# Kernel tuning notes

Hardware: AMD Instinct MI355X
Metric: run time of the kernel (lower is better)

The kernel has to match this reference:

```python
import jax, jax.numpy as jnp
import numpy as np

B, N, PLANE, H, W = 2, 6, 64, 48, 48
HIDP = 64
PS = 3
RATES = 3


def conv2d(x, w, b, pad, dil=1):
    # x: [BN, Cin, H, W], w: [Cout, Cin, kh, kw]
    out = jax.lax.conv_general_dilated(
        x, w, window_strides=(1, 1),
        padding=[(pad, pad), (pad, pad)],
        rhs_dilation=(dil, dil),
        dimension_numbers=('NCHW', 'OIHW', 'NCHW'))
    return out + b[None, :, None, None]


def avgpool3(x):
    bn, c, h, w = x.shape
    return x.reshape(bn, c, h // PS, PS, w // PS, PS).mean(axis=(3, 5))


def setup_inputs() -> dict:
    key = jax.random.key(0)
    ks = jax.random.split(key, 20)
    s = 0.05
    hid_pa = PLANE * 3  # 192, hidden width of MultiFieldConv2d
    d = {
        'x': jax.random.normal(ks[0], (B, N, PLANE, H, W), jnp.float32),
        # patch_aggr: 3 dilated convs (rates 1..3), k=3, plane -> plane*3
        'pa_w1': jax.random.normal(ks[1], (hid_pa, PLANE, 3, 3)) * s,
        'pa_b1': jnp.zeros((hid_pa,)),
        'pa_w2': jax.random.normal(ks[2], (hid_pa, PLANE, 3, 3)) * s,
        'pa_b2': jnp.zeros((hid_pa,)),
        'pa_w3': jax.random.normal(ks[3], (hid_pa, PLANE, 3, 3)) * s,
        'pa_b3': jnp.zeros((hid_pa,)),
        # convert: 1x1 (hid_pa*rates -> 3*hidp), relu, 1x1 (3*hidp -> 3*hidp)
        'pa_cw1': jax.random.normal(ks[4], (3 * HIDP, hid_pa * RATES, 1, 1)) * s,
        'pa_cb1': jnp.zeros((3 * HIDP,)),
        'pa_cw2': jax.random.normal(ks[5], (3 * HIDP, 3 * HIDP, 1, 1)) * s,
        'pa_cb2': jnp.zeros((3 * HIDP,)),
        # to_kv conv: k=3 pad=1, hidp -> hidp
        'kv_w': jax.random.normal(ks[6], (HIDP, HIDP, 3, 3)) * s,
        'kv_b': jnp.zeros((HIDP,)),
        # to_out: 1x1 hidp->plane, relu, 1x1 plane->plane, relu
        'out_w1': jax.random.normal(ks[7], (PLANE, HIDP, 1, 1)) * s,
        'out_b1': jnp.zeros((PLANE,)),
        'out_w2': jax.random.normal(ks[8], (PLANE, PLANE, 1, 1)) * s,
        'out_b2': jnp.zeros((PLANE,)),
        'scales': jnp.ones((N,)),
    }
    return d


def reference(x, pa_w1, pa_b1, pa_w2, pa_b2, pa_w3, pa_b3,
              pa_cw1, pa_cb1, pa_cw2, pa_cb2,
              kv_w, kv_b, out_w1, out_b1, out_w2, out_b2, scales):
    b, n, c, h, w = x.shape
    scale = HIDP ** (-0.5)
    xf = x.reshape(b * n, c, h, w)

    # MultiFieldConv2d: dilated convs (same spatial size for odd k), concat, 1x1 convert
    u = jnp.concatenate([
        conv2d(xf, pa_w1, pa_b1, pad=1, dil=1),
        conv2d(xf, pa_w2, pa_b2, pad=2, dil=2),
        conv2d(xf, pa_w3, pa_b3, pad=3, dil=3),
    ], axis=1)
    qkv = conv2d(jax.nn.relu(conv2d(u, pa_cw1, pa_cb1, 0)), pa_cw2, pa_cb2, 0)
    qkv = jax.nn.relu(qkv)  # F.relu(patch_aggr(x))
    xq, xk, xv = jnp.split(qkv, 3, axis=1)  # each [BN, hidp, H, W]

    def to_kv(t):
        return avgpool3(jax.nn.relu(conv2d(t, kv_w, kv_b, pad=PS // 2)))

    k_ = to_kv(xk)                       # [BN, hidp, H/3, W/3]
    v_ = to_kv(xv) * (1.0 / PS ** 2)

    hw_kv = k_.shape[2] * k_.shape[3]
    Qs = xq.reshape(b, n, HIDP, h * w).transpose(0, 1, 3, 2)   # b n g d
    Ks = k_.reshape(b, n, HIDP, hw_kv).transpose(0, 1, 3, 2)   # b m k d
    Vs = v_.reshape(b, n, HIDP, hw_kv).transpose(0, 1, 3, 2)

    # Leave-one-out sigmoid attention: sum_{j != i} sigmoid(q_i k_j^T * scale) @ v_j
    # Computed as full sum minus the self (j == i) term (exact same math).
    A_all = jax.nn.sigmoid(jnp.einsum('bngd,bmkd->bngmk', Qs, Ks) * scale)
    out_all = jnp.einsum('bngmk,bmkd->bngd', A_all, Vs)
    A_self = jax.nn.sigmoid(jnp.einsum('bngd,bnkd->bngk', Qs, Ks) * scale)
    out_self = jnp.einsum('bngk,bnkd->bngd', A_self, Vs)
    attn_out = out_all - out_self                               # [b, n, HW, hidp]

    res = attn_out.transpose(0, 1, 3, 2).reshape(b, n, HIDP, h, w)
    xv5 = xv.reshape(b, n, HIDP, h, w)
    res = jax.nn.relu(res + scales[None, :, None, None, None] * xv5)

    rf = res.reshape(b * n, HIDP, h, w)
    o = jax.nn.relu(conv2d(jax.nn.relu(conv2d(rf, out_w1, out_b1, 0)), out_w2, out_b2, 0))
    return o.reshape(b, n, c, h, w)
```

## Files before the change

kernel.cpp:

```cpp
#include <hip/hip_runtime.h>
#include <hip/hip_bf16.h>
#include <math.h>

#define BB 2
#define NVIEW 6
#define BN 12
#define CIN 64
#define HH 48
#define WW 48
#define PP (HH*WW)
#define OC 192
#define HPA 192
#define HIDP 64
#define KHW 16
#define PK 256
#define PADW 54
#define PADA (PADW*PADW)
#define NTOT (BN*PP)
#define K1 1728
#define KVPW 50
#define KVPA (KVPW*KVPW)

typedef __attribute__((ext_vector_type(8))) short bf16x8;
typedef __attribute__((ext_vector_type(4))) float f32x4;

#define OFF_WEFFB 0
#define SZ_WEFFB_FL (OC*K1/2)
#define OFF_BEFF (OFF_WEFFB + SZ_WEFFB_FL)
#define SZ_BEFF 256
#define OFF_CW2B (OFF_BEFF + SZ_BEFF)
#define SZ_CW2B_FL (OC*OC/2)
#define OFF_WKVB (OFF_CW2B + SZ_CW2B_FL)
#define SZ_WKVB_FL (64*576/2)
#define OFF_PADXT (OFF_WKVB + SZ_WKVB_FL)
#define SZ_PADXT_FL (BN*PADA*64/2)
#define OFF_QB16 (OFF_PADXT + SZ_PADXT_FL)
#define SZ_QB16_FL (BN*PP*64/2)
#define OFF_KB16 (OFF_QB16 + SZ_QB16_FL)
#define SZ_KB16_FL (BN*PK*64/2)
#define OFF_VB16T (OFF_KB16 + SZ_KB16_FL)
#define SZ_VB16T_FL (BN*64*PK/2)
#define OFF_KVPAD (OFF_VB16T + SZ_VB16T_FL)
#define SZ_KVPAD_FL (BN*2*KVPA*64/2)
#define OFF_CONVB (OFF_KVPAD + SZ_KVPAD_FL)
#define SZ_CONVB_FL (BN*2*PP*64/2)
#define OFF_W1SW (OFF_CONVB + SZ_CONVB_FL)
#define SZ_WSW_FL 2048
#define OFF_W2SW (OFF_W1SW + SZ_WSW_FL)
#define OFF_ATTNP (OFF_W2SW + SZ_WSW_FL)
#define SZ_ATTNP (BN*PP*HIDP)
#define OFF_XVB16 (OFF_ATTNP + 2*SZ_ATTNP)
#define SZ_XVB16_FL (BN*PP*64/2)

__device__ __forceinline__ void load_lds16(const void* g, void* l) {
    __builtin_amdgcn_global_load_lds(
        (const __attribute__((address_space(1))) unsigned int*)g,
        (__attribute__((address_space(3))) unsigned int*)l, 16, 0, 0);
}

__device__ __forceinline__ unsigned short f2bu(float f) {
    __hip_bfloat16 h = __float2bfloat16(f);
    return *(unsigned short*)&h;
}

__device__ __forceinline__ float bu2f(unsigned short h) {
    unsigned int u = ((unsigned int)h) << 16;
    return *(float*)&u;
}

__global__ __launch_bounds__(192) void k_fold(const float* __restrict__ cw1,
                       const float* __restrict__ cb1,
                       const float* __restrict__ w1, const float* __restrict__ b1,
                       const float* __restrict__ w2, const float* __restrict__ b2,
                       const float* __restrict__ w3, const float* __restrict__ b3,
                       __hip_bfloat16* __restrict__ weffb, float* __restrict__ beff) {
    __shared__ float cw1s[8][HPA];
    int b = blockIdx.x;
    int r = b / 72;
    int rem = b % 72;
    int og = rem / 3, tz = rem % 3;
    int tid = threadIdx.x;
    int tg = tz*192 + tid;
    int ic = tg / 9, tap = tg % 9;
    const float* w = (r==0) ? w1 : (r==1) ? w2 : w3;
    #pragma unroll
    for (int j = 0; j < 8; ++j)
        cw1s[j][tid] = cw1[(size_t)(og*8+j)*(HPA*3) + r*HPA + tid];
    __syncthreads();
    float acc[8] = {0,0,0,0,0,0,0,0};
    for (int c = 0; c < HPA; ++c) {
        float wv = w[(size_t)c*(CIN*9) + tg];
        #pragma unroll
        for (int j = 0; j < 8; ++j)
            acc[j] += cw1s[j][c] * wv;
    }
    #pragma unroll
    for (int j = 0; j < 8; ++j)
        weffb[(size_t)(og*8+j)*K1 + r*576 + tap*64 + ic] = __float2bfloat16(acc[j]);
    if (r == 0 && tz == 0 && tid < 8) {
        int o = og*8 + tid;
        float bacc = cb1[o];
        for (int rr = 0; rr < 3; ++rr) {
            const float* bb = (rr==0)?b1:(rr==1)?b2:b3;
            for (int c = 0; c < HPA; ++c)
                bacc += cw1[(size_t)o*(HPA*3) + rr*HPA + c] * bb[c];
        }
        beff[o] = bacc;
    }
}

__global__ void k_wprep(const float* __restrict__ kvw, const float* __restrict__ cw2,
                        const float* __restrict__ w1, const float* __restrict__ w2,
                        __hip_bfloat16* __restrict__ wkvb, __hip_bfloat16* __restrict__ cw2b,
                        __hip_bfloat16* __restrict__ w1sw, __hip_bfloat16* __restrict__ w2sw,
                        __hip_bfloat16* __restrict__ kvpad) {
    int idx = blockIdx.x*256 + threadIdx.x;
    if (idx < 36864) {
        int oc = idx / 576, rest = idx % 576;
        int tap = rest / 64, ic = rest % 64;
        wkvb[idx] = __float2bfloat16(kvw[(oc*64 + ic)*9 + tap]);
    } else if (idx < 73728) {
        int i = idx - 36864;
        cw2b[i] = __float2bfloat16(cw2[i]);
    } else if (idx < 81920) {
        int i = idx - 73728;
        const float* w = (i < 4096) ? w1 : w2;
        __hip_bfloat16* dst = (i < 4096) ? w1sw : w2sw;
        int j = i & 4095;
        int oc = j >> 6, s = (j >> 3) & 7, e = j & 7;
        int k = ((s ^ (oc & 7)) << 3) + e;
        dst[j] = __float2bfloat16(w[oc*64 + k]);
    } else if (idx < 86624) {
        int i = idx - 81920;
        int bn2 = i / 196, h = i % 196;
        int py, px;
        if (h < 50)       { py = 0;        px = h; }
        else if (h < 100) { py = 49;       px = h - 50; }
        else if (h < 148) { py = h - 99;   px = 0; }
        else              { py = h - 147;  px = 49; }
        bf16x8 z = (bf16x8){0,0,0,0,0,0,0,0};
        __hip_bfloat16* dst = kvpad + ((size_t)bn2*KVPA + py*KVPW + px)*64;
        #pragma unroll
        for (int j = 0; j < 8; ++j) *(bf16x8*)(dst + j*8) = z;
    }
}

__global__ void k_padxT(const float* __restrict__ x, __hip_bfloat16* __restrict__ padxT) {
    int idx = blockIdx.x*256 + threadIdx.x;
    if (idx >= BN*PADA) return;
    int spos = idx % PADA; int bn = idx / PADA;
    int sy = spos / PADW, sx = spos % PADW;
    __hip_bfloat16* dst = padxT + (size_t)idx*64;
    if (sy >= 3 && sy < 51 && sx >= 3 && sx < 51) {
        const float* src = x + (size_t)bn*CIN*PP + (sy-3)*WW + (sx-3);
        #pragma unroll 8
        for (int ic = 0; ic < 64; ++ic) dst[ic] = __float2bfloat16(src[ic*PP]);
    } else {
        #pragma unroll 8
        for (int ic = 0; ic < 64; ++ic) dst[ic] = __float2bfloat16(0.f);
    }
}

__global__ __launch_bounds__(256) void k_mfc(const __hip_bfloat16* __restrict__ wA,
        const __hip_bfloat16* __restrict__ pxT, const __hip_bfloat16* __restrict__ cw2b,
        const float* __restrict__ beff, const float* __restrict__ cb2,
        __hip_bfloat16* __restrict__ xvb16, __hip_bfloat16* __restrict__ qb16,
        __hip_bfloat16* __restrict__ kvpad) {
    __shared__ __align__(16) char smem[65536];
    int tid = threadIdx.x;
    int wid = tid >> 6, lane = tid & 63;
    int bn = blockIdx.x / 36;
    int pb = (blockIdx.x % 36) * 64;
    int sgr = ((lane&7) ^ (lane>>3)) * 8;
    int l7 = lane & 7, lh = lane >> 4, rrow = lane & 15, gcol = lane >> 4;

    size_t gbase[8];
    int dbase[8];
    #pragma unroll
    for (int s2 = 0; s2 < 8; ++s2) {
        int seg = wid*8 + s2;
        if (seg < 24) {
            int row = seg*8 + (lane>>3);
            gbase[s2] = (size_t)row*K1 + sgr;
            dbase[s2] = seg*1024;
        } else {
            int p = pb + (seg-24)*8 + (lane>>3);
            int py = p / WW, px = p % WW;
            gbase[s2] = ((size_t)bn*PADA + (py+3)*PADW + (px+3))*64 + sgr;
            dbase[s2] = 49152 + (seg-24)*1024;
        }
    }

    auto stage1 = [&](int kt, int par) {
        int r_ = kt / 9, tap = kt - r_*9;
        int doff = (r_+1)*((tap/3 - 1)*PADW + (tap%3 - 1));
        int poA = par ? 24576 : 0;
        int poB = par ? 8192 : 0;
        #pragma unroll
        for (int s2 = 0; s2 < 8; ++s2) {
            int seg = wid*8 + s2;
            const __hip_bfloat16* g = (seg < 24) ? wA + gbase[s2] + kt*64
                                                 : pxT + gbase[s2] + (size_t)doff*64;
            load_lds16(g, smem + dbase[s2] + ((seg < 24) ? poA : poB));
        }
    };

    f32x4 acc1[3][4];
    #pragma unroll
    for (int m = 0; m < 3; ++m)
        #pragma unroll
        for (int nf = 0; nf < 4; ++nf) acc1[m][nf] = (f32x4){0.f,0.f,0.f,0.f};

    stage1(0, 0);
    __syncthreads();
    for (int kt = 0; kt < 27; ++kt) {
        int par = kt & 1;
        if (kt < 26) stage1(kt+1, par^1);
        int aB = par ? 24576 : 0;
        int bB = 49152 + (par ? 8192 : 0);
        bf16x8 a[3][2], b[4][2];
        #pragma unroll
        for (int kk = 0; kk < 2; ++kk) {
            int gof = ((kk*4 + lh) ^ l7) << 4;
            #pragma unroll
            for (int m = 0; m < 3; ++m)
                a[m][kk] = *(const bf16x8*)(smem + aB + (wid*48 + m*16 + rrow)*128 + gof);
            #pragma unroll
            for (int nf = 0; nf < 4; ++nf)
                b[nf][kk] = *(const bf16x8*)(smem + bB + (nf*16 + rrow)*128 + gof);
        }
        #pragma unroll
        for (int kk = 0; kk < 2; ++kk)
            #pragma unroll
            for (int m = 0; m < 3; ++m)
                #pragma unroll
                for (int nf = 0; nf < 4; ++nf)
                    acc1[m][nf] = __builtin_amdgcn_mfma_f32_16x16x32_bf16(
                        a[m][kk], b[nf][kk], acc1[m][nf], 0, 0, 0);
        __syncthreads();
    }

    f32x4 acc2[3][4];
    #pragma unroll
    for (int m = 0; m < 3; ++m)
        #pragma unroll
        for (int nf = 0; nf < 4; ++nf) acc2[m][nf] = (f32x4){0.f,0.f,0.f,0.f};

    for (int kt2 = 0; kt2 < 3; ++kt2) {
        if (kt2) __syncthreads();
        #pragma unroll
        for (int s2 = 0; s2 < 6; ++s2) {
            int seg = wid*6 + s2;
            int row = seg*8 + (lane>>3);
            load_lds16(cw2b + (size_t)row*OC + kt2*64 + sgr, smem + seg*1024);
        }
        #pragma unroll
        for (int m = 0; m < 3; ++m) {
            int oc16 = wid*48 + m*16;
            if ((oc16 >> 6) == kt2) {
                int oc0 = oc16 + gcol*4;
                float4 bz = *(const float4*)&beff[oc0];
                int cb = (oc0 - kt2*64)*2;
                #pragma unroll
                for (int nf = 0; nf < 4; ++nf) {
                    int px = nf*16 + rrow;
                    ushort4 hv;
                    hv.x = f2bu(fmaxf(acc1[m][nf][0] + bz.x, 0.f));
                    hv.y = f2bu(fmaxf(acc1[m][nf][1] + bz.y, 0.f));
                    hv.z = f2bu(fmaxf(acc1[m][nf][2] + bz.z, 0.f));
                    hv.w = f2bu(fmaxf(acc1[m][nf][3] + bz.w, 0.f));
                    *(ushort4*)(smem + 49152 + px*136 + cb) = hv;
                }
            }
        }
        __syncthreads();
        #pragma unroll
        for (int kk = 0; kk < 2; ++kk) {
            int gofA = ((kk*4 + lh) ^ l7) << 4;
            int gofB = (kk*4 + lh) << 4;
            bf16x8 a2[3], b2[4];
            #pragma unroll
            for (int m2 = 0; m2 < 3; ++m2)
                a2[m2] = *(const bf16x8*)(smem + (wid*48 + m2*16 + rrow)*128 + gofA);
            #pragma unroll
            for (int nf = 0; nf < 4; ++nf)
                b2[nf] = *(const bf16x8*)(smem + 49152 + (nf*16 + rrow)*136 + gofB);
            #pragma unroll
            for (int m2 = 0; m2 < 3; ++m2)
                #pragma unroll
                for (int nf = 0; nf < 4; ++nf)
                    acc2[m2][nf] = __builtin_amdgcn_mfma_f32_16x16x32_bf16(
                        a2[m2], b2[nf], acc2[m2][nf], 0, 0, 0);
        }
    }

    #pragma unroll
    for (int m2 = 0; m2 < 3; ++m2) {
        int oc16 = wid*48 + m2*16;
        int sec = oc16 >> 6;
        int oc0 = oc16 + gcol*4;
        float4 cz = *(const float4*)&cb2[oc0];
        #pragma unroll
        for (int nf = 0; nf < 4; ++nf) {
            int px = nf*16 + rrow;
            int p = pb + px;
            ushort4 bv;
            bv.x = f2bu(fmaxf(acc2[m2][nf][0] + cz.x, 0.f));
            bv.y = f2bu(fmaxf(acc2[m2][nf][1] + cz.y, 0.f));
            bv.z = f2bu(fmaxf(acc2[m2][nf][2] + cz.z, 0.f));
            bv.w = f2bu(fmaxf(acc2[m2][nf][3] + cz.w, 0.f));
            if (sec == 0) {
                *(ushort4*)&qb16[((size_t)bn*PP + p)*64 + oc0] = bv;
            } else {
                int kv = sec - 1;
                int py = p / WW, pxx = p % WW;
                int d = oc0 - (sec << 6);
                *(ushort4*)&kvpad[((size_t)(bn*2+kv)*KVPA + (py+1)*KVPW + pxx+1)*64 + d] = bv;
                if (kv == 1)
                    *(ushort4*)&xvb16[((size_t)bn*PP + p)*64 + d] = bv;
            }
        }
    }
}

__global__ __launch_bounds__(256) void k_kvgemm(const __hip_bfloat16* __restrict__ wA,
        const __hip_bfloat16* __restrict__ kvpad, const float* __restrict__ kvb,
        __hip_bfloat16* __restrict__ convb) {
    __shared__ __align__(16) char smem[49152];
    int tid = threadIdx.x;
    int wid = tid >> 6, lane = tid & 63;
    int tileN = blockIdx.x * 128;
    int bn2 = tileN / PP, p0 = tileN % PP;
    int sgr = ((lane&7) ^ (lane>>3)) * 8;

    size_t gbase[6];
    #pragma unroll
    for (int s2 = 0; s2 < 6; ++s2) {
        int seg = wid*6 + s2;
        if (seg < 8) {
            int row = seg*8 + (lane>>3);
            gbase[s2] = (size_t)row*576 + sgr;
        } else {
            int p = p0 + (seg-8)*8 + (lane>>3);
            int py = p / WW, px = p % WW;
            gbase[s2] = ((size_t)bn2*KVPA + (py+1)*KVPW + px+1)*64 + sgr;
        }
    }
    auto stage2 = [&](int kt, int par) {
        int dy = kt/3 - 1, dx = kt%3 - 1;
        int doff = dy*KVPW + dx;
        #pragma unroll
        for (int s2 = 0; s2 < 6; ++s2) {
            int seg = wid*6 + s2;
            const __hip_bfloat16* g = (seg < 8) ? wA + gbase[s2] + kt*64
                                                : kvpad + gbase[s2] + (size_t)doff*64;
            load_lds16(g, smem + par*24576 + seg*1024);
        }
    };
    int wr = wid >> 1, wc = wid & 1;
    int l7 = lane & 7, lh = lane >> 4;
    int arowb[2], browb[4];
    #pragma unroll
    for (int m = 0; m < 2; ++m)
        arowb[m] = (wr*32 + m*16 + (lane&15))*128;
    #pragma unroll
    for (int nf = 0; nf < 4; ++nf)
        browb[nf] = 8192 + (wc*64 + nf*16 + (lane&15))*128;

    f32x4 acc[2][4];
    #pragma unroll
    for (int m = 0; m < 2; ++m)
        #pragma unroll
        for (int nf = 0; nf < 4; ++nf) acc[m][nf] = (f32x4){0.f,0.f,0.f,0.f};

    stage2(0, 0);
    __syncthreads();
    for (int kt = 0; kt < 9; ++kt) {
        int par = kt & 1;
        if (kt < 8) stage2(kt+1, par^1);
        int po = par*24576;
        bf16x8 a[2][2], b[4][2];
        #pragma unroll
        for (int kk = 0; kk < 2; ++kk) {
            int gof = ((kk*4 + lh) ^ l7) << 4;
            #pragma unroll
            for (int m = 0; m < 2; ++m)
                a[m][kk] = *(const bf16x8*)(smem + po + arowb[m] + gof);
            #pragma unroll
            for (int nf = 0; nf < 4; ++nf)
                b[nf][kk] = *(const bf16x8*)(smem + po + browb[nf] + gof);
        }
        #pragma unroll
        for (int kk = 0; kk < 2; ++kk)
            #pragma unroll
            for (int m = 0; m < 2; ++m)
                #pragma unroll
                for (int nf = 0; nf < 4; ++nf)
                    acc[m][nf] = __builtin_amdgcn_mfma_f32_16x16x32_bf16(
                        a[m][kk], b[nf][kk], acc[m][nf], 0, 0, 0);
        __syncthreads();
    }
    #pragma unroll
    for (int m = 0; m < 2; ++m) {
        int rbase = wr*32 + m*16 + (lane>>4)*4;
        float4 bz = *(const float4*)&kvb[rbase];
        #pragma unroll
        for (int nf = 0; nf < 4; ++nf) {
            int col = p0 + wc*64 + nf*16 + (lane&15);
            ushort4 cv;
            cv.x = f2bu(fmaxf(acc[m][nf][0] + bz.x, 0.f));
            cv.y = f2bu(fmaxf(acc[m][nf][1] + bz.y, 0.f));
            cv.z = f2bu(fmaxf(acc[m][nf][2] + bz.z, 0.f));
            cv.w = f2bu(fmaxf(acc[m][nf][3] + bz.w, 0.f));
            *(ushort4*)&convb[((size_t)bn2*PP + col)*64 + rbase] = cv;
        }
    }
}

__global__ __launch_bounds__(256) void k_pool(const __hip_bfloat16* __restrict__ convb,
        __hip_bfloat16* __restrict__ kbufb, __hip_bfloat16* __restrict__ vbufT) {
    int idx = blockIdx.x*256 + threadIdx.x;
    int dg = idx % 8; idx /= 8;
    int pp = idx % PK; idx /= PK;
    int bn2 = idx;
    int kv = bn2 & 1, bn = bn2 >> 1;
    int qy = pp / KHW, qx = pp % KHW;
    float s[8] = {0,0,0,0,0,0,0,0};
    const __hip_bfloat16* base = convb + (size_t)bn2*PP*64 + dg*8;
    #pragma unroll
    for (int sy = 0; sy < 3; ++sy)
        #pragma unroll
        for (int sx = 0; sx < 3; ++sx) {
            union { bf16x8 v; unsigned short h[8]; } c;
            c.v = *(const bf16x8*)(base + ((size_t)(qy*3+sy)*WW + qx*3+sx)*64);
            #pragma unroll
            for (int j = 0; j < 8; ++j) s[j] += bu2f(c.h[j]);
        }
    if (kv == 0) {
        union { ushort4 u[2]; unsigned short h[8]; } cv;
        #pragma unroll
        for (int j = 0; j < 8; ++j) cv.h[j] = f2bu(s[j] * (1.f/9.f));
        ushort4* dst = (ushort4*)(kbufb + ((size_t)bn*PK + pp)*64 + dg*8);
        dst[0] = cv.u[0]; dst[1] = cv.u[1];
    } else {
        #pragma unroll
        for (int j = 0; j < 8; ++j)
            vbufT[((size_t)bn*64 + dg*8 + j)*PK + pp] = __float2bfloat16(s[j]*(1.f/81.f));
    }
}

__global__ __launch_bounds__(256) void k_attn3(const __hip_bfloat16* __restrict__ qb16,
        const __hip_bfloat16* __restrict__ kbufb, const __hip_bfloat16* __restrict__ vbufT,
        float* __restrict__ attnp) {
    __shared__ __align__(16) char smem[32768];
    char* Qs = smem;
    char* Ks = smem + 8192;
    char* Vs = smem + 16384;
    char* Ps = smem + 24576;
    int tid = threadIdx.x;
    int wid = tid >> 6, lane = tid & 63;
    int bid = blockIdx.x;
    int ks = bid & 1; bid >>= 1;
    int qt = bid % 36; int bn = bid / 36;
    int b = bn / NVIEW, n = bn % NVIEW;
    int p0 = qt*64;

    {
        const char* gq = (const char*)(qb16 + ((size_t)bn*PP + p0)*64);
        #pragma unroll
        for (int i = 0; i < 2; ++i) {
            int s = wid*2 + i;
            int lin = s*1024 + lane*16;
            int r = lin >> 7, c = (lin >> 4) & 7;
            int gof = (r<<7) + ((c ^ (r&7)) << 4);
            load_lds16(gq + gof, Qs + s*1024);
        }
    }
    int arow = wid*16 + (lane&15);
    int brow = lane&15;
    int gcol = lane>>4;
    int vrow = tid >> 2;
    int vc2 = (tid & 3) * 2;

    f32x4 oacc[4];
    #pragma unroll
    for (int i = 0; i < 4; ++i) oacc[i] = (f32x4){0,0,0,0};

    for (int mi = 0; mi < NVIEW-1; ++mi) {
        int m = mi + (mi >= n ? 1 : 0);
        int bnk = b*NVIEW + m;
        const char* gk = (const char*)(kbufb + (size_t)bnk*PK*64);
        const __hip_bfloat16* gv = vbufT + (size_t)bnk*64*PK;
        for (int kc = ks*2; kc < ks*2+2; ++kc) {
            __syncthreads();
            #pragma unroll
            for (int i = 0; i < 2; ++i) {
                int s = wid*2 + i;
                int lin = s*1024 + lane*16;
                int r = lin >> 7, c = (lin >> 4) & 7;
                int gof = (r<<7) + ((c ^ (r&7)) << 4);
                load_lds16(gk + (size_t)kc*8192 + gof, Ks + s*1024);
            }
            {
                const __hip_bfloat16* src = gv + vrow*PK + kc*64 + vc2*8;
                bf16x8 v0 = *(const bf16x8*)src;
                bf16x8 v1 = *(const bf16x8*)(src+8);
                *(bf16x8*)(Vs + vrow*128 + ((vc2 ^ (vrow&7))<<4)) = v0;
                *(bf16x8*)(Vs + vrow*128 + (((vc2+1) ^ (vrow&7))<<4)) = v1;
            }
            __syncthreads();
            f32x4 sacc[4];
            #pragma unroll
            for (int i = 0; i < 4; ++i) sacc[i] = (f32x4){0,0,0,0};
            #pragma unroll
            for (int kk = 0; kk < 2; ++kk) {
                int g = kk*4 + gcol;
                bf16x8 af = *(const bf16x8*)(Ks + arow*128 + ((g ^ (arow&7))<<4));
                #pragma unroll
                for (int nf = 0; nf < 4; ++nf) {
                    int q = nf*16 + brow;
                    bf16x8 bq = *(const bf16x8*)(Qs + q*128 + ((g ^ (q&7))<<4));
                    sacc[nf] = __builtin_amdgcn_mfma_f32_16x16x32_bf16(af, bq, sacc[nf], 0,0,0);
                }
            }
            {
                int kbase = wid*16 + gcol*4;
                #pragma unroll
                for (int nf = 0; nf < 4; ++nf) {
                    int q = nf*16 + brow;
                    ushort4 pu;
                    float e0 = __expf(-sacc[nf][0]*0.125f);
                    float e1 = __expf(-sacc[nf][1]*0.125f);
                    float e2 = __expf(-sacc[nf][2]*0.125f);
                    float e3 = __expf(-sacc[nf][3]*0.125f);
                    pu.x = f2bu(__builtin_amdgcn_rcpf(1.f+e0));
                    pu.y = f2bu(__builtin_amdgcn_rcpf(1.f+e1));
                    pu.z = f2bu(__builtin_amdgcn_rcpf(1.f+e2));
                    pu.w = f2bu(__builtin_amdgcn_rcpf(1.f+e3));
                    *(ushort4*)(Ps + q*128 + (((kbase>>3) ^ (q&7))<<4) + (kbase&7)*2) = pu;
                }
            }
            __syncthreads();
            #pragma unroll
            for (int kk = 0; kk < 2; ++kk) {
                int g = kk*4 + gcol;
                int qr = wid*16 + brow;
                bf16x8 pf = *(const bf16x8*)(Ps + qr*128 + ((g ^ (qr&7))<<4));
                #pragma unroll
                for (int nf = 0; nf < 4; ++nf) {
                    int d = nf*16 + brow;
                    bf16x8 vf = *(const bf16x8*)(Vs + d*128 + ((g ^ (d&7))<<4));
                    oacc[nf] = __builtin_amdgcn_mfma_f32_16x16x32_bf16(pf, vf, oacc[nf], 0,0,0);
                }
            }
        }
    }
    float* ab = attnp + (size_t)ks*SZ_ATTNP + ((size_t)bn*PP + p0)*64;
    #pragma unroll
    for (int nf = 0; nf < 4; ++nf) {
        #pragma unroll
        for (int r = 0; r < 4; ++r) {
            int q = wid*16 + gcol*4 + r;
            int d = nf*16 + brow;
            ab[(size_t)q*64 + d] = oacc[nf][r];
        }
    }
}

__global__ __launch_bounds__(256) void k_out2(const float* __restrict__ attnp,
        const __hip_bfloat16* __restrict__ xvb16, const float* __restrict__ scales,
        const __hip_bfloat16* __restrict__ w1sw, const __hip_bfloat16* __restrict__ w2sw,
        const float* __restrict__ b1, const float* __restrict__ b2,
        float* __restrict__ out) {
    __shared__ __align__(16) char smem[49152];
    char* W1s = smem;
    char* W2s = smem + 8192;
    char* Rs  = smem + 16384;
    char* Ts  = smem + 32768;
    int tid = threadIdx.x;
    int wid = tid >> 6, lane = tid & 63;
    int pix0 = blockIdx.x * 128;
    int bn = pix0 / PP;
    int pb = pix0 - bn*PP;
    float sc = scales[bn % NVIEW];

    #pragma unroll
    for (int i = 0; i < 4; ++i) {
        int seg = wid*4 + i;
        const char* src = (seg < 8) ? (const char*)w1sw + seg*1024
                                    : (const char*)w2sw + (seg-8)*1024;
        load_lds16(src + lane*16, smem + seg*1024);
    }
    {
        int p = tid >> 1, d0 = (tid & 1) * 32;
        int P = pix0 + p;
        const float* a0 = attnp + (size_t)P*64 + d0;
        const float* a1 = a0 + SZ_ATTNP;
        const __hip_bfloat16* xv = xvb16 + (size_t)P*64 + d0;
        #pragma unroll
        for (int j = 0; j < 4; ++j) {
            float4 u0 = *(const float4*)(a0 + j*8);
            float4 u1 = *(const float4*)(a0 + j*8 + 4);
            float4 v0 = *(const float4*)(a1 + j*8);
            float4 v1 = *(const float4*)(a1 + j*8 + 4);
            union { bf16x8 v; unsigned short h[8]; } xu;
            xu.v = *(const bf16x8*)(xv + j*8);
            union { bf16x8 v; unsigned short h[8]; } rv;
            rv.h[0] = f2bu(fmaxf(u0.x + v0.x + sc*bu2f(xu.h[0]), 0.f));
            rv.h[1] = f2bu(fmaxf(u0.y + v0.y + sc*bu2f(xu.h[1]), 0.f));
            rv.h[2] = f2bu(fmaxf(u0.z + v0.z + sc*bu2f(xu.h[2]), 0.f));
            rv.h[3] = f2bu(fmaxf(u0.w + v0.w + sc*bu2f(xu.h[3]), 0.f));
            rv.h[4] = f2bu(fmaxf(u1.x + v1.x + sc*bu2f(xu.h[4]), 0.f));
            rv.h[5] = f2bu(fmaxf(u1.y + v1.y + sc*bu2f(xu.h[5]), 0.f));
            rv.h[6] = f2bu(fmaxf(u1.z + v1.z + sc*bu2f(xu.h[6]), 0.f));
            rv.h[7] = f2bu(fmaxf(u1.w + v1.w + sc*bu2f(xu.h[7]), 0.f));
            int g = (d0 >> 3) + j;
            *(bf16x8*)(Rs + p*128 + ((g ^ (p&7)) << 4)) = rv.v;
        }
    }
    __syncthreads();

    int wr = wid >> 1, wc = wid & 1;
    int rrow = lane & 15, gcol = lane >> 4;
    f32x4 acc1[2][4];
    #pragma unroll
    for (int m = 0; m < 2; ++m)
        #pragma unroll
        for (int nf = 0; nf < 4; ++nf) acc1[m][nf] = (f32x4){0,0,0,0};
    #pragma unroll
    for (int kk = 0; kk < 2; ++kk) {
        int g = kk*4 + gcol;
        #pragma unroll
        for (int m = 0; m < 2; ++m) {
            int oc = wr*32 + m*16 + rrow;
            bf16x8 af = *(const bf16x8*)(W1s + oc*128 + ((g ^ (oc&7)) << 4));
            #pragma unroll
            for (int nf = 0; nf < 4; ++nf) {
                int px = wc*64 + nf*16 + rrow;
                bf16x8 bf = *(const bf16x8*)(Rs + px*128 + ((g ^ (px&7)) << 4));
                acc1[m][nf] = __builtin_amdgcn_mfma_f32_16x16x32_bf16(af, bf, acc1[m][nf], 0,0,0);
            }
        }
    }
    #pragma unroll
    for (int m = 0; m < 2; ++m) {
        int oc0 = wr*32 + m*16 + gcol*4;
        float4 bz = *(const float4*)&b1[oc0];
        #pragma unroll
        for (int nf = 0; nf < 4; ++nf) {
            int px = wc*64 + nf*16 + rrow;
            ushort4 tv;
            tv.x = f2bu(fmaxf(acc1[m][nf][0] + bz.x, 0.f));
            tv.y = f2bu(fmaxf(acc1[m][nf][1] + bz.y, 0.f));
            tv.z = f2bu(fmaxf(acc1[m][nf][2] + bz.z, 0.f));
            tv.w = f2bu(fmaxf(acc1[m][nf][3] + bz.w, 0.f));
            *(ushort4*)(Ts + px*128 + (((oc0>>3) ^ (px&7)) << 4) + (oc0&7)*2) = tv;
        }
    }
    __syncthreads();
    f32x4 acc2[2][4];
    #pragma unroll
    for (int m = 0; m < 2; ++m)
        #pragma unroll
        for (int nf = 0; nf < 4; ++nf) acc2[m][nf] = (f32x4){0,0,0,0};
    #pragma unroll
    for (int kk = 0; kk < 2; ++kk) {
        int g = kk*4 + gcol;
        #pragma unroll
        for (int m = 0; m < 2; ++m) {
            int oc = wr*32 + m*16 + rrow;
            bf16x8 af = *(const bf16x8*)(W2s + oc*128 + ((g ^ (oc&7)) << 4));
            #pragma unroll
            for (int nf = 0; nf < 4; ++nf) {
                int px = wc*64 + nf*16 + rrow;
                bf16x8 bf = *(const bf16x8*)(Ts + px*128 + ((g ^ (px&7)) << 4));
                acc2[m][nf] = __builtin_amdgcn_mfma_f32_16x16x32_bf16(af, bf, acc2[m][nf], 0,0,0);
            }
        }
    }
    #pragma unroll
    for (int m = 0; m < 2; ++m) {
        int oc0 = wr*32 + m*16 + gcol*4;
        float4 bz = *(const float4*)&b2[oc0];
        #pragma unroll
        for (int nf = 0; nf < 4; ++nf) {
            int px = wc*64 + nf*16 + rrow;
            float* dst = out + ((size_t)bn*64 + oc0)*PP + pb + px;
            dst[0*PP] = fmaxf(acc2[m][nf][0] + bz.x, 0.f);
            dst[1*PP] = fmaxf(acc2[m][nf][1] + bz.y, 0.f);
            dst[2*PP] = fmaxf(acc2[m][nf][2] + bz.z, 0.f);
            dst[3*PP] = fmaxf(acc2[m][nf][3] + bz.w, 0.f);
        }
    }
}

extern "C" void kernel_launch(void* const* d_in, const int* in_sizes, int n_in,
                              void* d_out, int out_size, void* d_ws, size_t ws_size,
                              hipStream_t stream) {
    (void)in_sizes; (void)n_in; (void)out_size; (void)ws_size;
    const float* x      = (const float*)d_in[0];
    const float* pa_w1  = (const float*)d_in[1];
    const float* pa_b1  = (const float*)d_in[2];
    const float* pa_w2  = (const float*)d_in[3];
    const float* pa_b2  = (const float*)d_in[4];
    const float* pa_w3  = (const float*)d_in[5];
    const float* pa_b3  = (const float*)d_in[6];
    const float* pa_cw1 = (const float*)d_in[7];
    const float* pa_cb1 = (const float*)d_in[8];
    const float* pa_cw2 = (const float*)d_in[9];
    const float* pa_cb2 = (const float*)d_in[10];
    const float* kv_w   = (const float*)d_in[11];
    const float* kv_b   = (const float*)d_in[12];
    const float* out_w1 = (const float*)d_in[13];
    const float* out_b1 = (const float*)d_in[14];
    const float* out_w2 = (const float*)d_in[15];
    const float* out_b2 = (const float*)d_in[16];
    const float* scales = (const float*)d_in[17];
    float* out = (float*)d_out;
    float* ws  = (float*)d_ws;

    __hip_bfloat16* weffb = (__hip_bfloat16*)(ws + OFF_WEFFB);
    float* beff = ws + OFF_BEFF;
    __hip_bfloat16* cw2b  = (__hip_bfloat16*)(ws + OFF_CW2B);
    __hip_bfloat16* wkvb  = (__hip_bfloat16*)(ws + OFF_WKVB);
    __hip_bfloat16* padxT = (__hip_bfloat16*)(ws + OFF_PADXT);
    __hip_bfloat16* qb16  = (__hip_bfloat16*)(ws + OFF_QB16);
    __hip_bfloat16* kbufb = (__hip_bfloat16*)(ws + OFF_KB16);
    __hip_bfloat16* vbufT = (__hip_bfloat16*)(ws + OFF_VB16T);
    __hip_bfloat16* kvpad = (__hip_bfloat16*)(ws + OFF_KVPAD);
    __hip_bfloat16* convb = (__hip_bfloat16*)(ws + OFF_CONVB);
    __hip_bfloat16* w1sw  = (__hip_bfloat16*)(ws + OFF_W1SW);
    __hip_bfloat16* w2sw  = (__hip_bfloat16*)(ws + OFF_W2SW);
    float* attnp = ws + OFF_ATTNP;
    __hip_bfloat16* xvb16 = (__hip_bfloat16*)(ws + OFF_XVB16);

    k_fold<<<216, 192, 0, stream>>>(pa_cw1, pa_cb1, pa_w1, pa_b1,
                                    pa_w2, pa_b2, pa_w3, pa_b3, weffb, beff);
    k_wprep<<<339, 256, 0, stream>>>(kv_w, pa_cw2, out_w1, out_w2,
                                     wkvb, cw2b, w1sw, w2sw, kvpad);
    k_padxT<<<(BN*PADA+255)/256, 256, 0, stream>>>(x, padxT);
    k_mfc<<<NTOT/64, 256, 0, stream>>>(weffb, padxT, cw2b, beff, pa_cb2,
                                       xvb16, qb16, kvpad);
    k_kvgemm<<<BN*2*PP/128, 256, 0, stream>>>(wkvb, kvpad, kv_b, convb);
    k_pool<<<BN*2*PK*8/256, 256, 0, stream>>>(convb, kbufb, vbufT);
    k_attn3<<<BN*36*2, 256, 0, stream>>>(qb16, kbufb, vbufT, attnp);
    k_out2<<<NTOT/128, 256, 0, stream>>>(attnp, xvb16, scales, w1sw, w2sw,
                                         out_b1, out_b2, out);
}
```

Measured before the change: 113.5 us.

## Fuse attention with residual and output MLP, drop key-split partial buffers

The attention kernel now processes all four key chunks per block instead of splitting them across two blocks, then applies the scaled residual, ReLU and both 1x1 output convolutions in-kernel using LDS-resident weights. This removes the fp32 partial-sum buffers, their global write and reread, and one kernel launch. In exchange the grid is halved (432 to 216 blocks), which lowers parallelism on a large GPU, and LDS use per block grows.

```diff
diff --git a/kernel.cpp b/kernel.cpp
--- a/kernel.cpp
+++ b/kernel.cpp
@@ -47,9 +47,7 @@
 #define OFF_W1SW (OFF_CONVB + SZ_CONVB_FL)
 #define SZ_WSW_FL 2048
 #define OFF_W2SW (OFF_W1SW + SZ_WSW_FL)
-#define OFF_ATTNP (OFF_W2SW + SZ_WSW_FL)
-#define SZ_ATTNP (BN*PP*HIDP)
-#define OFF_XVB16 (OFF_ATTNP + 2*SZ_ATTNP)
+#define OFF_XVB16 (OFF_W2SW + SZ_WSW_FL)
 #define SZ_XVB16_FL (BN*PP*64/2)
 
 __device__ __forceinline__ void load_lds16(const void* g, void* l) {
@@ -449,24 +447,29 @@
     }
 }
 
-__global__ __launch_bounds__(256) void k_attn3(const __hip_bfloat16* __restrict__ qb16,
+__global__ __launch_bounds__(256) void k_attn4(const __hip_bfloat16* __restrict__ qb16,
         const __hip_bfloat16* __restrict__ kbufb, const __hip_bfloat16* __restrict__ vbufT,
-        float* __restrict__ attnp) {
-    __shared__ __align__(16) char smem[32768];
-    char* Qs = smem;
-    char* Ks = smem + 8192;
-    char* Vs = smem + 16384;
-    char* Ps = smem + 24576;
+        const __hip_bfloat16* __restrict__ xvb16, const float* __restrict__ scales,
+        const __hip_bfloat16* __restrict__ w1sw, const __hip_bfloat16* __restrict__ w2sw,
+        const float* __restrict__ b1, const float* __restrict__ b2,
+        float* __restrict__ out) {
+    __shared__ __align__(16) char smem[40960];
+    char* Qs  = smem;
+    char* Ks  = smem + 8192;
+    char* Vs  = smem + 16384;
+    char* Ps  = smem + 24576;
+    char* XVs = smem + 32768;
     int tid = threadIdx.x;
     int wid = tid >> 6, lane = tid & 63;
-    int bid = blockIdx.x;
-    int ks = bid & 1; bid >>= 1;
-    int qt = bid % 36; int bn = bid / 36;
+    int qt = blockIdx.x % 36;
+    int bn = blockIdx.x / 36;
     int b = bn / NVIEW, n = bn % NVIEW;
     int p0 = qt*64;
+    float sc = scales[n];
 
     {
-        const char* gq = (const char*)(qb16 + ((size_t)bn*PP + p0)*64);
+        const char* gq  = (const char*)(qb16  + ((size_t)bn*PP + p0)*64);
+        const char* gxv = (const char*)(xvb16 + ((size_t)bn*PP + p0)*64);
         #pragma unroll
         for (int i = 0; i < 2; ++i) {
             int s = wid*2 + i;
@@ -474,6 +477,7 @@
             int r = lin >> 7, c = (lin >> 4) & 7;
             int gof = (r<<7) + ((c ^ (r&7)) << 4);
             load_lds16(gq + gof, Qs + s*1024);
+            load_lds16(gxv + gof, XVs + s*1024);
         }
     }
     int arow = wid*16 + (lane&15);
@@ -491,7 +495,7 @@
         int bnk = b*NVIEW + m;
         const char* gk = (const char*)(kbufb + (size_t)bnk*PK*64);
         const __hip_bfloat16* gv = vbufT + (size_t)bnk*64*PK;
-        for (int kc = ks*2; kc < ks*2+2; ++kc) {
+        for (int kc = 0; kc < 4; ++kc) {
             __syncthreads();
             #pragma unroll
             for (int i = 0; i < 2; ++i) {
@@ -555,141 +559,83 @@
             }
         }
     }
-    float* ab = attnp + (size_t)ks*SZ_ATTNP + ((size_t)bn*PP + p0)*64;
-    #pragma unroll
-    for (int nf = 0; nf < 4; ++nf) {
-        #pragma unroll
-        for (int r = 0; r < 4; ++r) {
-            int q = wid*16 + gcol*4 + r;
-            int d = nf*16 + brow;
-            ab[(size_t)q*64 + d] = oacc[nf][r];
-        }
-    }
-}
-
-__global__ __launch_bounds__(256) void k_out2(const float* __restrict__ attnp,
-        const __hip_bfloat16* __restrict__ xvb16, const float* __restrict__ scales,
-        const __hip_bfloat16* __restrict__ w1sw, const __hip_bfloat16* __restrict__ w2sw,
-        const float* __restrict__ b1, const float* __restrict__ b2,
-        float* __restrict__ out) {
-    __shared__ __align__(16) char smem[49152];
-    char* W1s = smem;
-    char* W2s = smem + 8192;
-    char* Rs  = smem + 16384;
-    char* Ts  = smem + 32768;
-    int tid = threadIdx.x;
-    int wid = tid >> 6, lane = tid & 63;
-    int pix0 = blockIdx.x * 128;
-    int bn = pix0 / PP;
-    int pb = pix0 - bn*PP;
-    float sc = scales[bn % NVIEW];
-
+
+    __syncthreads();
     #pragma unroll
     for (int i = 0; i < 4; ++i) {
         int seg = wid*4 + i;
         const char* src = (seg < 8) ? (const char*)w1sw + seg*1024
                                     : (const char*)w2sw + (seg-8)*1024;
-        load_lds16(src + lane*16, smem + seg*1024);
-    }
-    {
-        int p = tid >> 1, d0 = (tid & 1) * 32;
-        int P = pix0 + p;
-        const float* a0 = attnp + (size_t)P*64 + d0;
-        const float* a1 = a0 + SZ_ATTNP;
-        const __hip_bfloat16* xv = xvb16 + (size_t)P*64 + d0;
-        #pragma unroll
-        for (int j = 0; j < 4; ++j) {
-            float4 u0 = *(const float4*)(a0 + j*8);
-            float4 u1 = *(const float4*)(a0 + j*8 + 4);
-            float4 v0 = *(const float4*)(a1 + j*8);
-            float4 v1 = *(const float4*)(a1 + j*8 + 4);
-            union { bf16x8 v; unsigned short h[8]; } xu;
-            xu.v = *(const bf16x8*)(xv + j*8);
-            union { bf16x8 v; unsigned short h[8]; } rv;
-            rv.h[0] = f2bu(fmaxf(u0.x + v0.x + sc*bu2f(xu.h[0]), 0.f));
-            rv.h[1] = f2bu(fmaxf(u0.y + v0.y + sc*bu2f(xu.h[1]), 0.f));
-            rv.h[2] = f2bu(fmaxf(u0.z + v0.z + sc*bu2f(xu.h[2]), 0.f));
-            rv.h[3] = f2bu(fmaxf(u0.w + v0.w + sc*bu2f(xu.h[3]), 0.f));
-            rv.h[4] = f2bu(fmaxf(u1.x + v1.x + sc*bu2f(xu.h[4]), 0.f));
-            rv.h[5] = f2bu(fmaxf(u1.y + v1.y + sc*bu2f(xu.h[5]), 0.f));
-            rv.h[6] = f2bu(fmaxf(u1.z + v1.z + sc*bu2f(xu.h[6]), 0.f));
-            rv.h[7] = f2bu(fmaxf(u1.w + v1.w + sc*bu2f(xu.h[7]), 0.f));
-            int g = (d0 >> 3) + j;
-            *(bf16x8*)(Rs + p*128 + ((g ^ (p&7)) << 4)) = rv.v;
+        load_lds16(src + lane*16, ((seg < 8) ? Vs : Ps) + (seg & 7)*1024);
+    }
+    #pragma unroll
+    for (int nf = 0; nf < 4; ++nf) {
+        int d = nf*16 + brow;
+        #pragma unroll
+        for (int r = 0; r < 4; ++r) {
+            int q = wid*16 + gcol*4 + r;
+            int off = q*128 + (((d>>3) ^ (q&7))<<4) + (d&7)*2;
+            float xv = bu2f(*(const unsigned short*)(XVs + off));
+            *(unsigned short*)(Ks + off) = f2bu(fmaxf(oacc[nf][r] + sc*xv, 0.f));
         }
     }
     __syncthreads();
-
-    int wr = wid >> 1, wc = wid & 1;
-    int rrow = lane & 15, gcol = lane >> 4;
-    f32x4 acc1[2][4];
-    #pragma unroll
-    for (int m = 0; m < 2; ++m)
-        #pragma unroll
-        for (int nf = 0; nf < 4; ++nf) acc1[m][nf] = (f32x4){0,0,0,0};
+    f32x4 acc1[4];
+    #pragma unroll
+    for (int nf = 0; nf < 4; ++nf) acc1[nf] = (f32x4){0,0,0,0};
     #pragma unroll
     for (int kk = 0; kk < 2; ++kk) {
         int g = kk*4 + gcol;
-        #pragma unroll
-        for (int m = 0; m < 2; ++m) {
-            int oc = wr*32 + m*16 + rrow;
-            bf16x8 af = *(const bf16x8*)(W1s + oc*128 + ((g ^ (oc&7)) << 4));
-            #pragma unroll
-            for (int nf = 0; nf < 4; ++nf) {
-                int px = wc*64 + nf*16 + rrow;
-                bf16x8 bf = *(const bf16x8*)(Rs + px*128 + ((g ^ (px&7)) << 4));
-                acc1[m][nf] = __builtin_amdgcn_mfma_f32_16x16x32_bf16(af, bf, acc1[m][nf], 0,0,0);
-            }
-        }
-    }
-    #pragma unroll
-    for (int m = 0; m < 2; ++m) {
-        int oc0 = wr*32 + m*16 + gcol*4;
+        int oc = wid*16 + brow;
+        bf16x8 af = *(const bf16x8*)(Vs + oc*128 + ((g ^ (oc&7)) << 4));
+        #pragma unroll
+        for (int nf = 0; nf < 4; ++nf) {
+            int px = nf*16 + brow;
+            bf16x8 bf = *(const bf16x8*)(Ks + px*128 + ((g ^ (px&7)) << 4));
+            acc1[nf] = __builtin_amdgcn_mfma_f32_16x16x32_bf16(af, bf, acc1[nf], 0,0,0);
+        }
+    }
+    {
+        int oc0 = wid*16 + gcol*4;
         float4 bz = *(const float4*)&b1[oc0];
         #pragma unroll
         for (int nf = 0; nf < 4; ++nf) {
-            int px = wc*64 + nf*16 + rrow;
+            int px = nf*16 + brow;
             ushort4 tv;
-            tv.x = f2bu(fmaxf(acc1[m][nf][0] + bz.x, 0.f));
-            tv.y = f2bu(fmaxf(acc1[m][nf][1] + bz.y, 0.f));
-            tv.z = f2bu(fmaxf(acc1[m][nf][2] + bz.z, 0.f));
-            tv.w = f2bu(fmaxf(acc1[m][nf][3] + bz.w, 0.f));
-            *(ushort4*)(Ts + px*128 + (((oc0>>3) ^ (px&7)) << 4) + (oc0&7)*2) = tv;
+            tv.x = f2bu(fmaxf(acc1[nf][0] + bz.x, 0.f));
+            tv.y = f2bu(fmaxf(acc1[nf][1] + bz.y, 0.f));
+            tv.z = f2bu(fmaxf(acc1[nf][2] + bz.z, 0.f));
+            tv.w = f2bu(fmaxf(acc1[nf][3] + bz.w, 0.f));
+            *(ushort4*)(XVs + px*128 + (((oc0>>3) ^ (px&7)) << 4) + (oc0&7)*2) = tv;
         }
     }
     __syncthreads();
-    f32x4 acc2[2][4];
-    #pragma unroll
-    for (int m = 0; m < 2; ++m)
-        #pragma unroll
-        for (int nf = 0; nf < 4; ++nf) acc2[m][nf] = (f32x4){0,0,0,0};
+    f32x4 acc2[4];
+    #pragma unroll
+    for (int nf = 0; nf < 4; ++nf) acc2[nf] = (f32x4){0,0,0,0};
     #pragma unroll
     for (int kk = 0; kk < 2; ++kk) {
         int g = kk*4 + gcol;
-        #pragma unroll
-        for (int m = 0; m < 2; ++m) {
-            int oc = wr*32 + m*16 + rrow;
-            bf16x8 af = *(const bf16x8*)(W2s + oc*128 + ((g ^ (oc&7)) << 4));
-            #pragma unroll
-            for (int nf = 0; nf < 4; ++nf) {
-                int px = wc*64 + nf*16 + rrow;
-                bf16x8 bf = *(const bf16x8*)(Ts + px*128 + ((g ^ (px&7)) << 4));
-                acc2[m][nf] = __builtin_amdgcn_mfma_f32_16x16x32_bf16(af, bf, acc2[m][nf], 0,0,0);
-            }
-        }
-    }
-    #pragma unroll
-    for (int m = 0; m < 2; ++m) {
-        int oc0 = wr*32 + m*16 + gcol*4;
+        int oc = wid*16 + brow;
+        bf16x8 af = *(const bf16x8*)(Ps + oc*128 + ((g ^ (oc&7)) << 4));
+        #pragma unroll
+        for (int nf = 0; nf < 4; ++nf) {
+            int px = nf*16 + brow;
+            bf16x8 bf = *(const bf16x8*)(XVs + px*128 + ((g ^ (px&7)) << 4));
+            acc2[nf] = __builtin_amdgcn_mfma_f32_16x16x32_bf16(af, bf, acc2[nf], 0,0,0);
+        }
+    }
+    {
+        int oc0 = wid*16 + gcol*4;
         float4 bz = *(const float4*)&b2[oc0];
         #pragma unroll
         for (int nf = 0; nf < 4; ++nf) {
-            int px = wc*64 + nf*16 + rrow;
-            float* dst = out + ((size_t)bn*64 + oc0)*PP + pb + px;
-            dst[0*PP] = fmaxf(acc2[m][nf][0] + bz.x, 0.f);
-            dst[1*PP] = fmaxf(acc2[m][nf][1] + bz.y, 0.f);
-            dst[2*PP] = fmaxf(acc2[m][nf][2] + bz.z, 0.f);
-            dst[3*PP] = fmaxf(acc2[m][nf][3] + bz.w, 0.f);
+            int px = nf*16 + brow;
+            float* dst = out + ((size_t)bn*64 + oc0)*PP + p0 + px;
+            dst[0*PP] = fmaxf(acc2[nf][0] + bz.x, 0.f);
+            dst[1*PP] = fmaxf(acc2[nf][1] + bz.y, 0.f);
+            dst[2*PP] = fmaxf(acc2[nf][2] + bz.z, 0.f);
+            dst[3*PP] = fmaxf(acc2[nf][3] + bz.w, 0.f);
         }
     }
 }
@@ -731,7 +677,6 @@
     __hip_bfloat16* convb = (__hip_bfloat16*)(ws + OFF_CONVB);
     __hip_bfloat16* w1sw  = (__hip_bfloat16*)(ws + OFF_W1SW);
     __hip_bfloat16* w2sw  = (__hip_bfloat16*)(ws + OFF_W2SW);
-    float* attnp = ws + OFF_ATTNP;
     __hip_bfloat16* xvb16 = (__hip_bfloat16*)(ws + OFF_XVB16);
 
     k_fold<<<216, 192, 0, stream>>>(pa_cw1, pa_cb1, pa_w1, pa_b1,
@@ -743,7 +688,6 @@
                                        xvb16, qb16, kvpad);
     k_kvgemm<<<BN*2*PP/128, 256, 0, stream>>>(wkvb, kvpad, kv_b, convb);
     k_pool<<<BN*2*PK*8/256, 256, 0, stream>>>(convb, kbufb, vbufT);
-    k_attn3<<<BN*36*2, 256, 0, stream>>>(qb16, kbufb, vbufT, attnp);
-    k_out2<<<NTOT/128, 256, 0, stream>>>(attnp, xvb16, scales, w1sw, w2sw,
-                                         out_b1, out_b2, out);
-}
+    k_attn4<<<BN*36, 256, 0, stream>>>(qb16, kbufb, vbufT, xvb16, scales,
+                                       w1sw, w2sw, out_b1, out_b2, out);
+}
```

New measurement: 111.5 us, median of 2. Within noise of the previous version (-1.7%).
